# Kernel optimization log

Measured on AMD Instinct MI355X. Metric: run time of the kernel, lower is better.

## Reference

```python
import jax, jax.numpy as jnp
import numpy as np

DIM = 512
N_HEADS = 8
N_KV_HEADS = 4
HEAD_DIM = DIM // N_HEADS  # 64
N_REP = N_HEADS // N_KV_HEADS  # 2
THETA = 10000.0
EPS_RMS = 1e-6
EPS_Z = 1e-6


def setup_inputs() -> dict:
    key = jax.random.key(0)
    ks = jax.random.split(key, 6)
    s = 1.0 / np.sqrt(DIM)
    return {
        "x": jax.random.normal(ks[0], (4, 8192, DIM), dtype=jnp.float32),
        "norm_w": jnp.ones((DIM,), dtype=jnp.float32),
        "wq": jax.random.normal(ks[1], (DIM, DIM), dtype=jnp.float32) * s,
        "wk": jax.random.normal(ks[2], (N_KV_HEADS * HEAD_DIM, DIM), dtype=jnp.float32) * s,
        "wv": jax.random.normal(ks[3], (N_KV_HEADS * HEAD_DIM, DIM), dtype=jnp.float32) * s,
        "wo": jax.random.normal(ks[4], (DIM, DIM), dtype=jnp.float32) * s,
    }


def _rope_cos_sin(seq_len, head_dim):
    # freqs_cis = polar(1, t * theta^(-2i/d))
    inv = 1.0 / (THETA ** (jnp.arange(0, head_dim, 2, dtype=jnp.float32) / head_dim))
    ang = jnp.arange(seq_len, dtype=jnp.float32)[:, None] * inv[None, :]  # (S, d/2)
    return jnp.cos(ang), jnp.sin(ang)


def _apply_rope(t, cos, sin):
    # t: (B, S, H, d); complex rotation on consecutive pairs
    B, S, H, d = t.shape
    tr = t.reshape(B, S, H, d // 2, 2)
    xr, xi = tr[..., 0], tr[..., 1]
    c = cos[None, :, None, :]  # (1, S, 1, d/2)
    s = sin[None, :, None, :]
    out = jnp.stack([xr * c - xi * s, xr * s + xi * c], axis=-1)
    return out.reshape(B, S, H, d)


def _forward(x, norm_w, wq, wk, wv, wo):
    B, S, _ = x.shape
    # RMSNorm
    x = x * jax.lax.rsqrt(jnp.mean(x * x, axis=-1, keepdims=True) + EPS_RMS) * norm_w
    xq = (x @ wq.T).reshape(B, S, N_HEADS, HEAD_DIM)
    xk = (x @ wk.T).reshape(B, S, N_KV_HEADS, HEAD_DIM)
    xv = (x @ wv.T).reshape(B, S, N_KV_HEADS, HEAD_DIM)
    cos, sin = _rope_cos_sin(S, HEAD_DIM)
    xq = _apply_rope(xq, cos, sin)
    xk = _apply_rope(xk, cos, sin)
    # repeat_kv: (B,S,Hkv,d) -> (B,S,Hkv*n_rep,d)
    keys = jnp.repeat(xk, N_REP, axis=2)
    values = jnp.repeat(xv, N_REP, axis=2)
    # to (B, H, S, d)
    Q = jnp.transpose(xq, (0, 2, 1, 3))
    K = jnp.transpose(keys, (0, 2, 1, 3))
    V = jnp.transpose(values, (0, 2, 1, 3))
    phi = lambda t: jax.nn.elu(t) + 1.0
    Q_lin, K_lin = phi(Q), phi(K)
    # Faithful to source: elementwise product reduced over s -> (B,H,d)
    KV = jnp.einsum('bhsd,bhsd->bhd', K_lin, V)
    K_sum = K_lin.sum(axis=2)  # (B,H,d)
    Z = jnp.einsum('bhsd,bhd->bhs', Q_lin, K_sum)[..., None]  # (B,H,S,1)
    Y = Q_lin * KV[:, :, None, :] / (Z + EPS_Z)  # (B,H,S,d)
    Y = jnp.transpose(Y, (0, 2, 1, 3)).reshape(B, S, N_HEADS * HEAD_DIM)
    return Y @ wo.T


def reference(x, norm_w, wq, wk, wv, wo):
    return _forward(x, norm_w, wq, wk, wv, wo)
```

## Files before the change

### kernel.cpp

```cpp
#include <hip/hip_runtime.h>
#include <cmath>

typedef __attribute__((ext_vector_type(8))) short short8;
typedef __attribute__((ext_vector_type(4))) float floatx4;

#define T_TOK 32768
#define DIMK 512

__device__ __forceinline__ unsigned short f2bf(float f) {
  union { float f; unsigned int u; } v; v.f = f;
  unsigned int r = (v.u + 0x7fffu + ((v.u >> 16) & 1u)) >> 16;
  return (unsigned short)r;
}
__device__ __forceinline__ float bf2f(unsigned short h) {
  union { unsigned int u; float f; } v; v.u = ((unsigned int)h) << 16;
  return v.f;
}

__device__ __forceinline__ void gload_lds16(const unsigned short* g, unsigned short* ldsbase) {
  __builtin_amdgcn_global_load_lds(
      (const __attribute__((address_space(1))) unsigned int*)g,
      (__attribute__((address_space(3))) unsigned int*)ldsbase, 16, 0, 0);
}

__global__ __launch_bounds__(256) void k_prep(const float* __restrict__ x,
    const float* __restrict__ norm_w, const float* __restrict__ wq,
    const float* __restrict__ wk, const float* __restrict__ wv,
    const float* __restrict__ wo, unsigned short* __restrict__ Wb,
    unsigned short* __restrict__ wob, float2* __restrict__ rope,
    float* __restrict__ KVz, unsigned short* __restrict__ xn) {
  if (blockIdx.x < 2048) {
    int i = blockIdx.x * 256 + threadIdx.x;
    float v;
    if (i < 262144) v = wq[i];
    else if (i < 393216) v = wk[i - 262144];
    else v = wv[i - 393216];
    Wb[i] = f2bf(v);
    if (i < 262144) {
      wob[i] = f2bf(wo[i]);
      int s = i >> 5, m = i & 31;
      const double c0 = 0.74989420933245582;
      double c1 = c0 * c0, c2 = c1 * c1, c3 = c2 * c2, c4 = c3 * c3;
      double p = 1.0;
      if (m & 1)  p *= c0;
      if (m & 2)  p *= c1;
      if (m & 4)  p *= c2;
      if (m & 8)  p *= c3;
      if (m & 16) p *= c4;
      double ang = (double)s * p;
      const double TWO_PI = 6.2831853071795864769;
      double q = rint(ang * (1.0 / TWO_PI));
      double r = fma(-q, TWO_PI, ang);
      float rf = (float)r;
      rope[i] = make_float2(cosf(rf), sinf(rf));
    }
    if (i < 2048) KVz[i] = 0.f;
  } else {
    int bid = blockIdx.x - 2048;
    int wave = threadIdx.x >> 6, lane = threadIdx.x & 63;
    size_t t = (size_t)bid * 4 + wave;
    const float4* xr = (const float4*)(x + t * DIMK);
    float4 a = xr[lane * 2];
    float4 b = xr[lane * 2 + 1];
    float ss = a.x * a.x + a.y * a.y + a.z * a.z + a.w * a.w
             + b.x * b.x + b.y * b.y + b.z * b.z + b.w * b.w;
    #pragma unroll
    for (int off = 32; off >= 1; off >>= 1) ss += __shfl_xor(ss, off, 64);
    float scale = rsqrtf(ss * (1.0f / DIMK) + 1e-6f);
    const float4* wr = (const float4*)norm_w;
    float4 w0 = wr[lane * 2], w1 = wr[lane * 2 + 1];
    uint4 o;
    o.x = (unsigned int)f2bf(a.x * scale * w0.x) | ((unsigned int)f2bf(a.y * scale * w0.y) << 16);
    o.y = (unsigned int)f2bf(a.z * scale * w0.z) | ((unsigned int)f2bf(a.w * scale * w0.w) << 16);
    o.z = (unsigned int)f2bf(b.x * scale * w1.x) | ((unsigned int)f2bf(b.y * scale * w1.y) << 16);
    o.w = (unsigned int)f2bf(b.z * scale * w1.z) | ((unsigned int)f2bf(b.w * scale * w1.w) << 16);
    *(uint4*)(xn + t * DIMK + lane * 8) = o;
  }
}

template <bool BF16_OUT>
__global__ __launch_bounds__(512, 2) void k_gemm256(const unsigned short* __restrict__ A,
    const unsigned short* __restrict__ Bw, void* __restrict__ Cv, int N) {
  constexpr int K = DIMK;
  extern __shared__ __align__(16) unsigned short smem[];
  unsigned short* const AsP = smem;
  unsigned short* const BsP = smem + 32768;

  const int tid = threadIdx.x;
  const int wave = tid >> 6, lane = tid & 63;
  const int r = lane & 15, quad = lane >> 4, r7 = r & 7;
  const int wm = (wave >> 2) * 128, wn = (wave & 3) * 64;

  const int nwg = gridDim.x * gridDim.y;
  const int bid = blockIdx.x + gridDim.x * blockIdx.y;
  const int cpx = nwg >> 3;
  const int nid = (bid & 7) * cpx + (bid >> 3);
  const int m0 = (nid & 127) * 256;
  const int n0 = (nid >> 7) * 256;

  const int srow = lane >> 3;
  const int scb = (lane & 7) ^ srow;
  const unsigned short* const Asrc = A + (size_t)(m0 + wave * 8 + srow) * K + scb * 8;
  const unsigned short* const Bsrc = Bw + (size_t)(n0 + wave * 8 + srow) * K + scb * 8;
  unsigned short* const Adst = AsP + wave * 8 * 64;
  unsigned short* const Bdst = BsP + wave * 8 * 64;

#define STAGE_A(buf, h, kt) do { \
    gload_lds16(Asrc + (size_t)((h) * 128) * K + (kt) * 64, Adst + (buf) * 16384 + ((h) * 128) * 64); \
    gload_lds16(Asrc + (size_t)((h) * 128 + 64) * K + (kt) * 64, Adst + (buf) * 16384 + ((h) * 128 + 64) * 64); \
  } while (0)
#define STAGE_B(buf, h, kt) do { \
    gload_lds16(Bsrc + (size_t)((h) * 128) * K + (kt) * 64, Bdst + (buf) * 16384 + ((h) * 128) * 64); \
    gload_lds16(Bsrc + (size_t)((h) * 128 + 64) * K + (kt) * 64, Bdst + (buf) * 16384 + ((h) * 128 + 64) * 64); \
  } while (0)

  short8 af[4][2], b0[2][2], b1[2][2];
  floatx4 acc[8][4];
  #pragma unroll
  for (int i = 0; i < 8; i++)
    #pragma unroll
    for (int j = 0; j < 4; j++)
      acc[i][j] = (floatx4){0.f, 0.f, 0.f, 0.f};

#define LDA8(buf, ah) do { \
    _Pragma("unroll") for (int ii = 0; ii < 4; ii++) \
      _Pragma("unroll") for (int kk = 0; kk < 2; kk++) \
        af[ii][kk] = *(const short8*)&AsP[(buf) * 16384 + (wm + (ah) * 64 + ii * 16 + r) * 64 + ((kk * 4 + quad) ^ r7) * 8]; \
  } while (0)
#define LDB4(buf, bh, arr) do { \
    _Pragma("unroll") for (int jj = 0; jj < 2; jj++) \
      _Pragma("unroll") for (int kk = 0; kk < 2; kk++) \
        arr[jj][kk] = *(const short8*)&BsP[(buf) * 16384 + (wn + (bh) * 32 + jj * 16 + r) * 64 + ((kk * 4 + quad) ^ r7) * 8]; \
  } while (0)
#define MFMAQ(ah, bh, arr) do { \
    __builtin_amdgcn_s_setprio(1); \
    _Pragma("unroll") for (int ii = 0; ii < 4; ii++) \
      _Pragma("unroll") for (int jj = 0; jj < 2; jj++) \
        _Pragma("unroll") for (int kk = 0; kk < 2; kk++) \
          acc[(ah) * 4 + ii][(bh) * 2 + jj] = __builtin_amdgcn_mfma_f32_16x16x32_bf16( \
              af[ii][kk], arr[jj][kk], acc[(ah) * 4 + ii][(bh) * 2 + jj], 0, 0, 0); \
    __builtin_amdgcn_s_setprio(0); \
  } while (0)
#define BAR() do { asm volatile("" ::: "memory"); __builtin_amdgcn_s_barrier(); asm volatile("" ::: "memory"); } while (0)
#define VMW(n) do { asm volatile("s_waitcnt vmcnt(" #n ")" ::: "memory"); __builtin_amdgcn_sched_barrier(0); } while (0)

  STAGE_A(0, 0, 0); STAGE_B(0, 0, 0); STAGE_A(0, 1, 0); STAGE_B(0, 1, 0);
  STAGE_A(1, 0, 1); STAGE_B(1, 0, 1); STAGE_A(1, 1, 1); STAGE_B(1, 1, 1);
  VMW(8);
  BAR();

  #pragma unroll
  for (int it = 0; it < 3; ++it) {
    const int kt = it * 2;
    LDA8(0, 0); LDB4(0, 0, b0);
    BAR(); MFMAQ(0, 0, b0); BAR();
    LDB4(0, 1, b1);
    BAR(); MFMAQ(0, 1, b1); BAR();
    LDA8(0, 1); STAGE_B(0, 0, kt + 2); STAGE_B(0, 1, kt + 2);
    BAR(); MFMAQ(1, 1, b1); BAR();
    STAGE_A(0, 0, kt + 2); STAGE_A(0, 1, kt + 2);
    BAR(); MFMAQ(1, 0, b0); VMW(8); BAR();
    LDA8(1, 0); LDB4(1, 0, b0);
    BAR(); MFMAQ(0, 0, b0); BAR();
    LDB4(1, 1, b1);
    BAR(); MFMAQ(0, 1, b1); BAR();
    LDA8(1, 1); STAGE_B(1, 0, kt + 3); STAGE_B(1, 1, kt + 3);
    BAR(); MFMAQ(1, 1, b1); BAR();
    STAGE_A(1, 0, kt + 3); STAGE_A(1, 1, kt + 3);
    BAR(); MFMAQ(1, 0, b0); VMW(8); BAR();
  }

  LDA8(0, 0); LDB4(0, 0, b0);
  BAR(); MFMAQ(0, 0, b0); BAR();
  LDB4(0, 1, b1);
  BAR(); MFMAQ(0, 1, b1); BAR();
  LDA8(0, 1);
  BAR(); MFMAQ(1, 1, b1); BAR();
  MFMAQ(1, 0, b0); VMW(0); BAR();
  LDA8(1, 0); LDB4(1, 0, b0);
  BAR(); MFMAQ(0, 0, b0); BAR();
  LDB4(1, 1, b1);
  BAR(); MFMAQ(0, 1, b1); BAR();
  LDA8(1, 1);
  BAR(); MFMAQ(1, 1, b1); BAR();
  MFMAQ(1, 0, b0);

  #pragma unroll
  for (int i = 0; i < 8; i++)
    #pragma unroll
    for (int j = 0; j < 4; j++) {
      int row = m0 + wm + i * 16 + quad * 4;
      int col = n0 + wn + j * 16 + r;
      #pragma unroll
      for (int p = 0; p < 4; p++) {
        if constexpr (BF16_OUT) {
          ((unsigned short*)Cv)[(size_t)(row + p) * N + col] = f2bf(acc[i][j][p]);
        } else {
          ((float*)Cv)[(size_t)(row + p) * N + col] = acc[i][j][p];
        }
      }
    }
#undef STAGE_A
#undef STAGE_B
#undef LDA8
#undef LDB4
#undef MFMAQ
#undef BAR
#undef VMW
}

__global__ __launch_bounds__(256) void k_kvred(const unsigned short* __restrict__ qkv,
    const float2* __restrict__ rope, float* __restrict__ KV, float* __restrict__ Ksum) {
  int bk = blockIdx.y;
  int b = bk >> 2, kh = bk & 3;
  int tid = threadIdx.x;
  int m = tid & 31;
  int sl = tid >> 5;
  int s0 = blockIdx.x * 256;
  float kvr = 0.f, kvi = 0.f, ksr = 0.f, ksi = 0.f;
  for (int si = sl; si < 256; si += 8) {
    int s = s0 + si;
    size_t t = (size_t)b * 8192 + s;
    const unsigned short* base = qkv + t * 1024;
    unsigned int kp = *(const unsigned int*)(base + 512 + kh * 64 + 2 * m);
    unsigned int vp = *(const unsigned int*)(base + 768 + kh * 64 + 2 * m);
    float kx = bf2f((unsigned short)(kp & 0xffffu));
    float ky = bf2f((unsigned short)(kp >> 16));
    float vx = bf2f((unsigned short)(vp & 0xffffu));
    float vy = bf2f((unsigned short)(vp >> 16));
    float2 cs = rope[s * 32 + m];
    float kr = kx * cs.x - ky * cs.y;
    float ki = kx * cs.y + ky * cs.x;
    kr = kr > 0.f ? kr + 1.f : __expf(kr);
    ki = ki > 0.f ? ki + 1.f : __expf(ki);
    kvr += kr * vx; kvi += ki * vy;
    ksr += kr;      ksi += ki;
  }
  __shared__ float red[256 * 4];
  red[tid * 4 + 0] = kvr; red[tid * 4 + 1] = kvi;
  red[tid * 4 + 2] = ksr; red[tid * 4 + 3] = ksi;
  __syncthreads();
  if (sl == 0) {
    for (int q = 1; q < 8; q++) {
      kvr += red[(q * 32 + m) * 4 + 0]; kvi += red[(q * 32 + m) * 4 + 1];
      ksr += red[(q * 32 + m) * 4 + 2]; ksi += red[(q * 32 + m) * 4 + 3];
    }
    atomicAdd(&KV[bk * 64 + 2 * m], kvr);
    atomicAdd(&KV[bk * 64 + 2 * m + 1], kvi);
    atomicAdd(&Ksum[bk * 64 + 2 * m], ksr);
    atomicAdd(&Ksum[bk * 64 + 2 * m + 1], ksi);
  }
}

__global__ __launch_bounds__(256) void k_qkern(const unsigned short* __restrict__ qkv,
    const float2* __restrict__ rope, const float* __restrict__ KV,
    const float* __restrict__ Ksum, unsigned short* __restrict__ Yb) {
  const int h = threadIdx.x >> 5;
  const int pr = threadIdx.x & 31;
  for (int t = blockIdx.x; t < T_TOK; t += gridDim.x) {
    int b = t >> 13, pos = t & 8191;
    unsigned int qp = *(const unsigned int*)(qkv + (size_t)t * 1024 + h * 64 + 2 * pr);
    float qx = bf2f((unsigned short)(qp & 0xffffu));
    float qy = bf2f((unsigned short)(qp >> 16));
    float2 cs = rope[pos * 32 + pr];
    float ar = qx * cs.x - qy * cs.y;
    float ai = qx * cs.y + qy * cs.x;
    ar = ar > 0.f ? ar + 1.f : __expf(ar);
    ai = ai > 0.f ? ai + 1.f : __expf(ai);
    int bk = b * 4 + (h >> 1);
    float2 ks = *(const float2*)(Ksum + bk * 64 + 2 * pr);
    float z = ar * ks.x + ai * ks.y;
    #pragma unroll
    for (int off = 16; off >= 1; off >>= 1) z += __shfl_xor(z, off, 64);
    float2 kv = *(const float2*)(KV + bk * 64 + 2 * pr);
    float inv = 1.0f / (z + 1e-6f);
    unsigned int o = (unsigned int)f2bf(ar * kv.x * inv)
                   | ((unsigned int)f2bf(ai * kv.y * inv) << 16);
    *(unsigned int*)(Yb + (size_t)t * 512 + h * 64 + 2 * pr) = o;
  }
}

extern "C" void kernel_launch(void* const* d_in, const int* in_sizes, int n_in,
                              void* d_out, int out_size, void* d_ws, size_t ws_size,
                              hipStream_t stream) {
  const float* x = (const float*)d_in[0];
  const float* norm_w = (const float*)d_in[1];
  const float* wq = (const float*)d_in[2];
  const float* wk = (const float*)d_in[3];
  const float* wv = (const float*)d_in[4];
  const float* wo = (const float*)d_in[5];
  float* out = (float*)d_out;

  char* ws = (char*)d_ws;
  unsigned short* xn  = (unsigned short*)(ws);
  unsigned short* Wb  = (unsigned short*)(ws + 33554432);
  unsigned short* wob = (unsigned short*)(ws + 34603008);
  unsigned short* qkv = (unsigned short*)(ws + 35127296);
  float2* rope        = (float2*)(ws + 102236160);
  float* KV           = (float*)(ws + 104333312);
  float* Ksum         = (float*)(ws + 104337408);
  unsigned short* Yb  = (unsigned short*)(ws + 104341504);

  static bool s_attr = false;
  if (!s_attr) {
    (void)hipFuncSetAttribute(reinterpret_cast<const void*>(&k_gemm256<true>),
                              hipFuncAttributeMaxDynamicSharedMemorySize, 131072);
    (void)hipFuncSetAttribute(reinterpret_cast<const void*>(&k_gemm256<false>),
                              hipFuncAttributeMaxDynamicSharedMemorySize, 131072);
    s_attr = true;
  }

  k_prep<<<10240, 256, 0, stream>>>(x, norm_w, wq, wk, wv, wo, Wb, wob, rope, KV, xn);
  k_gemm256<true><<<dim3(128, 4), 512, 131072, stream>>>(xn, Wb, (void*)qkv, 1024);
  k_kvred<<<dim3(32, 16), 256, 0, stream>>>(qkv, rope, KV, Ksum);
  k_qkern<<<4096, 256, 0, stream>>>(qkv, rope, KV, Ksum, Yb);
  k_gemm256<false><<<dim3(128, 2), 512, 131072, stream>>>(Yb, wob, (void*)out, 512);
}
```

Before: 227.1 us.

## Fuse K/V RoPE, feature map and KV reduction into QKV GEMM epilogue

Interleaves K and V weight rows per KV head so each 256-wide N tile of the QKV GEMM holds matching K and V columns. The epilogue for those tiles applies RoPE and ELU+1 to K, multiplies by V staged through shared memory, and atomically accumulates KV and Ksum, so K/V never go to global memory. This removes the separate k_kvred pass and halves the qkv write traffic. It also changes the tile-to-XCD mapping so N tiles of the same M rows share an XCD. The cost is a heavier GEMM epilogue with extra syncs, exps and atomics per block.

```diff
diff --git a/kernel.cpp b/kernel.cpp
--- a/kernel.cpp
+++ b/kernel.cpp
@@ -32,9 +32,14 @@
   if (blockIdx.x < 2048) {
     int i = blockIdx.x * 256 + threadIdx.x;
     float v;
-    if (i < 262144) v = wq[i];
-    else if (i < 393216) v = wk[i - 262144];
-    else v = wv[i - 393216];
+    if (i < 262144) {
+      v = wq[i];
+    } else {
+      int R = i >> 9, col = i & 511;
+      int h = (R - 512) >> 7, rem = (R - 512) & 127;
+      if (rem < 64) v = wk[(h * 64 + rem) * 512 + col];
+      else          v = wv[(h * 64 + rem - 64) * 512 + col];
+    }
     Wb[i] = f2bf(v);
     if (i < 262144) {
       wob[i] = f2bf(wo[i]);
@@ -78,9 +83,10 @@
   }
 }
 
-template <bool BF16_OUT>
+template <bool BF16_OUT, bool FUSE>
 __global__ __launch_bounds__(512, 2) void k_gemm256(const unsigned short* __restrict__ A,
-    const unsigned short* __restrict__ Bw, void* __restrict__ Cv, int N) {
+    const unsigned short* __restrict__ Bw, void* __restrict__ Cv, int ldc,
+    const float2* __restrict__ rope, float* __restrict__ KV, float* __restrict__ Ksum) {
   constexpr int K = DIMK;
   extern __shared__ __align__(16) unsigned short smem[];
   unsigned short* const AsP = smem;
@@ -91,12 +97,15 @@
   const int r = lane & 15, quad = lane >> 4, r7 = r & 7;
   const int wm = (wave >> 2) * 128, wn = (wave & 3) * 64;
 
-  const int nwg = gridDim.x * gridDim.y;
+  const int ngy = gridDim.y;
   const int bid = blockIdx.x + gridDim.x * blockIdx.y;
-  const int cpx = nwg >> 3;
-  const int nid = (bid & 7) * cpx + (bid >> 3);
-  const int m0 = (nid & 127) * 256;
-  const int n0 = (nid >> 7) * 256;
+  const int xcd = bid & 7;
+  const int j = bid >> 3;
+  const int lg = (ngy == 4) ? 2 : 1;
+  const int per = (gridDim.x * ngy) >> (3 + lg);
+  const int mt = xcd * per + (j >> lg);
+  const int nt = j & (ngy - 1);
+  const int m0 = mt * 256, n0 = nt * 256;
 
   const int srow = lane >> 3;
   const int scb = (lane & 7) ^ srow;
@@ -119,8 +128,8 @@
   #pragma unroll
   for (int i = 0; i < 8; i++)
     #pragma unroll
-    for (int j = 0; j < 4; j++)
-      acc[i][j] = (floatx4){0.f, 0.f, 0.f, 0.f};
+    for (int jj = 0; jj < 4; jj++)
+      acc[i][jj] = (floatx4){0.f, 0.f, 0.f, 0.f};
 
 #define LDA8(buf, ah) do { \
     _Pragma("unroll") for (int ii = 0; ii < 4; ii++) \
@@ -185,21 +194,76 @@
   BAR(); MFMAQ(1, 1, b1); BAR();
   MFMAQ(1, 0, b0);
 
-  #pragma unroll
-  for (int i = 0; i < 8; i++)
-    #pragma unroll
-    for (int j = 0; j < 4; j++) {
-      int row = m0 + wm + i * 16 + quad * 4;
-      int col = n0 + wn + j * 16 + r;
+  if (FUSE && n0 >= 512) {
+    const int b = m0 >> 13;
+    const int kh = ((n0 - 512) >> 8) * 2 + (wn >> 7);
+    const int hvb = (wn >> 7) << 6;
+    float* const Vs = (float*)smem;
+    __syncthreads();
+    if (wn & 64) {
       #pragma unroll
-      for (int p = 0; p < 4; p++) {
-        if constexpr (BF16_OUT) {
-          ((unsigned short*)Cv)[(size_t)(row + p) * N + col] = f2bf(acc[i][j][p]);
-        } else {
-          ((float*)Cv)[(size_t)(row + p) * N + col] = acc[i][j][p];
+      for (int i = 0; i < 8; i++)
+        #pragma unroll
+        for (int j2 = 0; j2 < 4; j2++)
+          #pragma unroll
+          for (int p = 0; p < 4; p++) {
+            int t = wm + i * 16 + quad * 4 + p;
+            Vs[t * 128 + hvb + j2 * 16 + r] = acc[i][j2][p];
+          }
+    }
+    __syncthreads();
+    if (!(wn & 64)) {
+      float kvp[4] = {0.f, 0.f, 0.f, 0.f};
+      float ksp[4] = {0.f, 0.f, 0.f, 0.f};
+      #pragma unroll
+      for (int i = 0; i < 8; i++)
+        #pragma unroll
+        for (int p = 0; p < 4; p++) {
+          int t = wm + i * 16 + quad * 4 + p;
+          int pos = (m0 + t) & 8191;
+          #pragma unroll
+          for (int j2 = 0; j2 < 4; j2++) {
+            float v = acc[i][j2][p];
+            float vp = __shfl_xor(v, 1, 64);
+            int d = j2 * 16 + r;
+            float2 cs = rope[pos * 32 + (d >> 1)];
+            float rk = (r & 1) ? (vp * cs.y + v * cs.x) : (v * cs.x - vp * cs.y);
+            rk = rk > 0.f ? rk + 1.f : __expf(rk);
+            kvp[j2] += rk * Vs[t * 128 + hvb + d];
+            ksp[j2] += rk;
+          }
+        }
+      #pragma unroll
+      for (int j2 = 0; j2 < 4; j2++) {
+        kvp[j2] += __shfl_xor(kvp[j2], 16, 64); kvp[j2] += __shfl_xor(kvp[j2], 32, 64);
+        ksp[j2] += __shfl_xor(ksp[j2], 16, 64); ksp[j2] += __shfl_xor(ksp[j2], 32, 64);
+      }
+      if (lane < 16) {
+        int base = (b * 4 + kh) * 64 + r;
+        #pragma unroll
+        for (int j2 = 0; j2 < 4; j2++) {
+          atomicAdd(&KV[base + j2 * 16], kvp[j2]);
+          atomicAdd(&Ksum[base + j2 * 16], ksp[j2]);
         }
       }
     }
+  } else {
+    #pragma unroll
+    for (int i = 0; i < 8; i++)
+      #pragma unroll
+      for (int j2 = 0; j2 < 4; j2++) {
+        int row = m0 + wm + i * 16 + quad * 4;
+        int col = n0 + wn + j2 * 16 + r;
+        #pragma unroll
+        for (int p = 0; p < 4; p++) {
+          if constexpr (BF16_OUT) {
+            ((unsigned short*)Cv)[(size_t)(row + p) * ldc + col] = f2bf(acc[i][j2][p]);
+          } else {
+            ((float*)Cv)[(size_t)(row + p) * ldc + col] = acc[i][j2][p];
+          }
+        }
+      }
+  }
 #undef STAGE_A
 #undef STAGE_B
 #undef LDA8
@@ -209,49 +273,6 @@
 #undef VMW
 }
 
-__global__ __launch_bounds__(256) void k_kvred(const unsigned short* __restrict__ qkv,
-    const float2* __restrict__ rope, float* __restrict__ KV, float* __restrict__ Ksum) {
-  int bk = blockIdx.y;
-  int b = bk >> 2, kh = bk & 3;
-  int tid = threadIdx.x;
-  int m = tid & 31;
-  int sl = tid >> 5;
-  int s0 = blockIdx.x * 256;
-  float kvr = 0.f, kvi = 0.f, ksr = 0.f, ksi = 0.f;
-  for (int si = sl; si < 256; si += 8) {
-    int s = s0 + si;
-    size_t t = (size_t)b * 8192 + s;
-    const unsigned short* base = qkv + t * 1024;
-    unsigned int kp = *(const unsigned int*)(base + 512 + kh * 64 + 2 * m);
-    unsigned int vp = *(const unsigned int*)(base + 768 + kh * 64 + 2 * m);
-    float kx = bf2f((unsigned short)(kp & 0xffffu));
-    float ky = bf2f((unsigned short)(kp >> 16));
-    float vx = bf2f((unsigned short)(vp & 0xffffu));
-    float vy = bf2f((unsigned short)(vp >> 16));
-    float2 cs = rope[s * 32 + m];
-    float kr = kx * cs.x - ky * cs.y;
-    float ki = kx * cs.y + ky * cs.x;
-    kr = kr > 0.f ? kr + 1.f : __expf(kr);
-    ki = ki > 0.f ? ki + 1.f : __expf(ki);
-    kvr += kr * vx; kvi += ki * vy;
-    ksr += kr;      ksi += ki;
-  }
-  __shared__ float red[256 * 4];
-  red[tid * 4 + 0] = kvr; red[tid * 4 + 1] = kvi;
-  red[tid * 4 + 2] = ksr; red[tid * 4 + 3] = ksi;
-  __syncthreads();
-  if (sl == 0) {
-    for (int q = 1; q < 8; q++) {
-      kvr += red[(q * 32 + m) * 4 + 0]; kvi += red[(q * 32 + m) * 4 + 1];
-      ksr += red[(q * 32 + m) * 4 + 2]; ksi += red[(q * 32 + m) * 4 + 3];
-    }
-    atomicAdd(&KV[bk * 64 + 2 * m], kvr);
-    atomicAdd(&KV[bk * 64 + 2 * m + 1], kvi);
-    atomicAdd(&Ksum[bk * 64 + 2 * m], ksr);
-    atomicAdd(&Ksum[bk * 64 + 2 * m + 1], ksi);
-  }
-}
-
 __global__ __launch_bounds__(256) void k_qkern(const unsigned short* __restrict__ qkv,
     const float2* __restrict__ rope, const float* __restrict__ KV,
     const float* __restrict__ Ksum, unsigned short* __restrict__ Yb) {
@@ -259,7 +280,7 @@
   const int pr = threadIdx.x & 31;
   for (int t = blockIdx.x; t < T_TOK; t += gridDim.x) {
     int b = t >> 13, pos = t & 8191;
-    unsigned int qp = *(const unsigned int*)(qkv + (size_t)t * 1024 + h * 64 + 2 * pr);
+    unsigned int qp = *(const unsigned int*)(qkv + (size_t)t * 512 + h * 64 + 2 * pr);
     float qx = bf2f((unsigned short)(qp & 0xffffu));
     float qy = bf2f((unsigned short)(qp >> 16));
     float2 cs = rope[pos * 32 + pr];
@@ -303,16 +324,17 @@
 
   static bool s_attr = false;
   if (!s_attr) {
-    (void)hipFuncSetAttribute(reinterpret_cast<const void*>(&k_gemm256<true>),
+    (void)hipFuncSetAttribute(reinterpret_cast<const void*>(&k_gemm256<true, true>),
                               hipFuncAttributeMaxDynamicSharedMemorySize, 131072);
-    (void)hipFuncSetAttribute(reinterpret_cast<const void*>(&k_gemm256<false>),
+    (void)hipFuncSetAttribute(reinterpret_cast<const void*>(&k_gemm256<false, false>),
                               hipFuncAttributeMaxDynamicSharedMemorySize, 131072);
     s_attr = true;
   }
 
   k_prep<<<10240, 256, 0, stream>>>(x, norm_w, wq, wk, wv, wo, Wb, wob, rope, KV, xn);
-  k_gemm256<true><<<dim3(128, 4), 512, 131072, stream>>>(xn, Wb, (void*)qkv, 1024);
-  k_kvred<<<dim3(32, 16), 256, 0, stream>>>(qkv, rope, KV, Ksum);
+  k_gemm256<true, true><<<dim3(128, 4), 512, 131072, stream>>>(
+      xn, Wb, (void*)qkv, 512, rope, KV, Ksum);
   k_qkern<<<4096, 256, 0, stream>>>(qkv, rope, KV, Ksum, Yb);
-  k_gemm256<false><<<dim3(128, 2), 512, 131072, stream>>>(Yb, wob, (void*)out, 512);
-}
+  k_gemm256<false, false><<<dim3(128, 2), 512, 131072, stream>>>(
+      Yb, wob, (void*)out, 512, nullptr, nullptr, nullptr);
+}
```

Result: faster. 220.3 us (-3.0%).
